# Kernel tuning notes

Hardware: AMD Instinct MI355X
Metric: run time of the kernel (lower is better)

## Reference

```python
import jax, jax.numpy as jnp
import numpy as np

EMBED = 50
SEQ = 100
NLABEL = 15
HID = 20
VOCAB = 50000
BATCH = 8192


def gru_scan(xs, W, U, b, return_sequences):
    """Keras GRUCell (reset_after=True, gate order z,r,h).
    xs: (B, T, D). W: (D, 3H), U: (H, 3H), b: (2, 3H) [input bias, recurrent bias].
    """
    B = xs.shape[0]
    H = U.shape[0]
    bi, br = b[0], b[1]
    h0 = jnp.zeros((B, H), dtype=xs.dtype)

    def step(h, x_t):
        mx = x_t @ W + bi                      # (B, 3H)
        mh = h @ U + br                        # (B, 3H)
        xz, xr, xh = mx[:, :H], mx[:, H:2*H], mx[:, 2*H:]
        hz, hr, hh_ = mh[:, :H], mh[:, H:2*H], mh[:, 2*H:]
        z = jax.nn.sigmoid(xz + hz)
        r = jax.nn.sigmoid(xr + hr)
        hh = jnp.tanh(xh + r * hh_)
        h_new = z * h + (1.0 - z) * hh
        return h_new, h_new

    xs_t = jnp.swapaxes(xs, 0, 1)              # (T, B, D)
    h_last, hs = jax.lax.scan(step, h0, xs_t)
    if return_sequences:
        return jnp.swapaxes(hs, 0, 1)          # (B, T, H)
    return h_last                               # (B, H)


def setup_inputs() -> dict:
    key = jax.random.key(0)
    ks = jax.random.split(key, 9)
    s = 0.05
    return {
        "x": jax.random.randint(ks[0], (BATCH, SEQ), 0, VOCAB),
        "emb_table": jax.random.normal(ks[1], (VOCAB, EMBED), jnp.float32) * s,
        "W1": jax.random.normal(ks[2], (EMBED, 3 * HID), jnp.float32) * s,
        "U1": jax.random.normal(ks[3], (HID, 3 * HID), jnp.float32) * s,
        "b1": jnp.zeros((2, 3 * HID), jnp.float32),
        "W2": jax.random.normal(ks[4], (HID, 3 * HID), jnp.float32) * s,
        "U2": jax.random.normal(ks[5], (HID, 3 * HID), jnp.float32) * s,
        "b2": jnp.zeros((2, 3 * HID), jnp.float32),
        "Wd": jax.random.normal(ks[6], (HID, NLABEL), jnp.float32) * s,
        "bd": jnp.zeros((NLABEL,), jnp.float32),
        "drop_rate": 0,
    }


def reference(x, emb_table, W1, U1, b1, W2, U2, b2, Wd, bd, drop_rate):
    emb = emb_table[x]                               # (B, T, E)
    seq = gru_scan(emb, W1, U1, b1, return_sequences=True)   # (B, T, H)
    enc = gru_scan(seq, W2, U2, b2, return_sequences=False)  # (B, H)
    # drop_rate == 0 -> tf.nn.dropout is identity
    logits = enc @ Wd + bd                           # (B, 15)
    return logits
```

## Files before the change

### kernel.cpp

```cpp
#include <hip/hip_runtime.h>
#include <hip/hip_bf16.h>
#include <hip/hip_fp16.h>

#define SEQ_T 100
#define HID 20
#define EMB_D 50
#define VOCAB_N 50000
#define TABW 60
#define NTILE 3125
#define BBLK 782

typedef short sh8 __attribute__((ext_vector_type(8)));
typedef float f4  __attribute__((ext_vector_type(4)));

#define OFF_U1P 0
#define OFF_W2P 600
#define OFF_U2P 1200
#define OFF_B1  3600
#define OFF_B2  3720
#define OFF_WD  3840
#define OFF_BD  4140
#define OFF_TAB 4160

__device__ __forceinline__ float ldf(const void* p, int i, int isf) {
  return isf ? ((const float*)p)[i]
             : __bfloat162float(((const __hip_bfloat16*)p)[i]);
}
__device__ __forceinline__ short f2bf(float f) {
  unsigned u = __float_as_uint(f);
  u += 0x7fffu + ((u >> 16) & 1u);
  return (short)(u >> 16);
}
__device__ __forceinline__ float rdl(float v, int l) {
  return __uint_as_float(__builtin_amdgcn_readlane(__float_as_uint(v), l));
}
__device__ __forceinline__ int detect_isf(const void* emb) {
  uint4 dv = ((const uint4*)emb)[threadIdx.x & 63];
  int big = 0;
#pragma unroll
  for (int i = 0; i < 4; ++i) {
    unsigned w = ((const unsigned*)&dv)[i];
    big |= (((w >> 7) & 0xFF) >= 140) | (((w >> 23) & 0xFF) >= 140);
  }
  return (__ballot(big) != 0ull) ? 1 : 0;
}

__global__ __launch_bounds__(256) void build_table(
    const void* __restrict__ emb, const void* __restrict__ W1,
    const void* __restrict__ b1,
    const void* __restrict__ U1, const void* __restrict__ W2,
    const void* __restrict__ U2, const void* __restrict__ b2,
    const void* __restrict__ Wd, const void* __restrict__ bd,
    float* __restrict__ ws)
{
  const int isf = detect_isf(emb);
  if (blockIdx.x == 0) {
    const int t = threadIdx.x;
    unsigned* wsu = (unsigned*)ws;
    for (int i = t; i < 600; i += 256) {
      const int j = i / 10, p = i % 10;
      const int k0 = 2 * p, k1 = 2 * p + 1;
#define PK(M) ((unsigned)__half_as_ushort(__float2half_rn(ldf(M, k0 * 60 + j, isf))) | \
               ((unsigned)__half_as_ushort(__float2half_rn(ldf(M, k1 * 60 + j, isf))) << 16))
      wsu[OFF_U1P + i] = PK(U1);
      wsu[OFF_W2P + i] = PK(W2);
      wsu[OFF_U2P + i] = PK(U2);
#undef PK
    }
    for (int i = t; i < 120; i += 256) {
      ws[OFF_B1 + i] = ldf(b1, i, isf);
      ws[OFF_B2 + i] = ldf(b2, i, isf);
    }
    for (int i = t; i < 300; i += 256) ws[OFF_WD + i] = ldf(Wd, i, isf);
    for (int i = t; i < 15;  i += 256) ws[OFF_BD + i] = ldf(bd, i, isf);
  }

  const int L = threadIdx.x & 63, q = L >> 4, c = L & 15;
  const int wid = blockIdx.x * 4 + (threadIdx.x >> 6);
  float* __restrict__ tab = ws + OFF_TAB;

  __shared__ int4 sB[64][8];
  if (threadIdx.x < 64) {
#pragma unroll
    for (int nt = 0; nt < 4; ++nt) {
      const int col = nt * 16 + c;
      sh8 B0, B1;
#pragma unroll
      for (int jj = 0; jj < 8; ++jj) {
        const int k0 = q * 8 + jj, k1 = 32 + q * 8 + jj;
        B0[jj] = (col < TABW) ? f2bf(ldf(W1, k0 * TABW + col, isf)) : (short)0;
        B1[jj] = (col < TABW && k1 < EMB_D)
                     ? f2bf(ldf(W1, k1 * TABW + col, isf)) : (short)0;
      }
      sB[L][nt * 2]     = *(const int4*)&B0;
      sB[L][nt * 2 + 1] = *(const int4*)&B1;
    }
  }
  float bi[4];
#pragma unroll
  for (int nt = 0; nt < 4; ++nt) {
    const int col = nt * 16 + c;
    bi[nt] = (col < TABW) ? ldf(b1, col, isf) : 0.f;
  }
  __syncthreads();

  for (int tile = wid; tile < NTILE; tile += BBLK * 4) {
    const int v0 = tile * 16;
    sh8 A0, A1;
#pragma unroll
    for (int jj = 0; jj < 8; ++jj) { A0[jj] = 0; A1[jj] = 0; }
    if (!isf) {
      const unsigned short* eb = (const unsigned short*)emb;
      const size_t rb = (size_t)(v0 + c) * EMB_D;
#pragma unroll
      for (int i = 0; i < 4; ++i) {
        unsigned d = *(const unsigned*)(eb + rb + q * 8 + 2 * i);
        A0[2 * i] = (short)(d & 0xffff); A0[2 * i + 1] = (short)(d >> 16);
      }
      const int k1b = 32 + q * 8;
#pragma unroll
      for (int i = 0; i < 4; ++i) {
        const int k = k1b + 2 * i;
        if (k + 1 < EMB_D) {
          unsigned d = *(const unsigned*)(eb + rb + k);
          A1[2 * i] = (short)(d & 0xffff); A1[2 * i + 1] = (short)(d >> 16);
        }
      }
    } else {
      const float* ef = (const float*)emb;
      const size_t rb = (size_t)(v0 + c) * EMB_D;
#pragma unroll
      for (int jj = 0; jj < 8; ++jj) {
        const int k0 = q * 8 + jj, k1 = 32 + q * 8 + jj;
        A0[jj] = f2bf(ef[rb + k0]);
        A1[jj] = (k1 < EMB_D) ? f2bf(ef[rb + k1]) : (short)0;
      }
    }
#pragma unroll
    for (int nt = 0; nt < 4; ++nt) {
      int4 b0i = sB[L][nt * 2], b1i = sB[L][nt * 2 + 1];
      sh8 B0 = *(const sh8*)&b0i, B1 = *(const sh8*)&b1i;
      const int col = nt * 16 + c;
      f4 acc = { bi[nt], bi[nt], bi[nt], bi[nt] };
      acc = __builtin_amdgcn_mfma_f32_16x16x32_bf16(A0, B0, acc, 0, 0, 0);
      acc = __builtin_amdgcn_mfma_f32_16x16x32_bf16(A1, B1, acc, 0, 0, 0);
      if (col < TABW) {
#pragma unroll
        for (int r = 0; r < 4; ++r)
          tab[(size_t)(v0 + q * 4 + r) * TABW + col] = acc[r];
      }
    }
  }
}

__global__ __launch_bounds__(256, 8) void gru_main(
    const int* __restrict__ x, const float* __restrict__ ws,
    const void* __restrict__ emb, void* __restrict__ out)
{
  const int isf = detect_isf(emb);
  const int j = threadIdx.x & 63;
  const int e = __builtin_amdgcn_readfirstlane(blockIdx.x * 4 + (threadIdx.x >> 6));
  const int jc = j < TABW ? j : 0;

  const int* xr = x + (size_t)e * SEQ_T;
  const float* tab = ws + OFF_TAB;
  const int o1 = jc * 40;
  const int jc4 = jc * 4;
  const int a1 = ((j - 20) & 63) * 4;
  const int a2 = ((j + 40) & 63) * 4;
  const float br1 = ws[OFF_B1 + 60 + jc];
  const float bi2 = ws[OFF_B2 + jc];
  const float br2 = ws[OFF_B2 + 60 + jc];
  float h2out;

  asm volatile(
    "global_load_dwordx4 v[10:13], %[o1], %[wsp] offset:0\n\t"
    "global_load_dwordx4 v[14:17], %[o1], %[wsp] offset:16\n\t"
    "global_load_dwordx2 v[18:19], %[o1], %[wsp] offset:32\n\t"
    "v_add_u32 v44, 0x960, %[o1]\n\t"
    "v_add_u32 v45, 0x12c0, %[o1]\n\t"
    "global_load_dwordx4 v[20:23], v44, %[wsp] offset:0\n\t"
    "global_load_dwordx4 v[24:27], v44, %[wsp] offset:16\n\t"
    "global_load_dwordx2 v[28:29], v44, %[wsp] offset:32\n\t"
    "global_load_dwordx4 v[30:33], v45, %[wsp] offset:0\n\t"
    "global_load_dwordx4 v[34:37], v45, %[wsp] offset:16\n\t"
    "global_load_dwordx2 v[38:39], v45, %[wsp] offset:32\n\t"
    "s_mov_b64 s[20:21], 0\n\ts_mov_b64 s[22:23], 0\n\t"
    "s_mov_b64 s[24:25], 0\n\ts_mov_b64 s[26:27], 0\n\t"
    "s_mov_b64 s[28:29], 0\n\t"
    "s_mov_b64 s[30:31], 0\n\ts_mov_b64 s[32:33], 0\n\t"
    "s_mov_b64 s[34:35], 0\n\ts_mov_b64 s[36:37], 0\n\t"
    "s_mov_b64 s[38:39], 0\n\t"
    "v_mov_b32 v40, 0\n\t"
    "v_mov_b32 v41, 0\n\t"
    "s_load_dword s65, %[xp], 0x0\n\t"
    "s_load_dword s66, %[xp], 0x4\n\t"
    "s_waitcnt lgkmcnt(0)\n\t"
    "s_mul_i32 s65, s65, 240\n\t"
    "s_mul_i32 s66, s66, 240\n\t"
    "v_add_u32 v50, s65, %[jc4]\n\t"
    "global_load_dword v42, v50, %[tabp]\n\t"
    "v_add_u32 v50, s66, %[jc4]\n\t"
    "global_load_dword v43, v50, %[tabp]\n\t"
    "s_load_dword s65, %[xp], 0x8\n\t"
    "s_movk_i32 s64, 0xc\n\t"
    "s_movk_i32 s67, 0x64\n\t"
    "s_waitcnt vmcnt(0)\n\t"
    "0:\n\t"
    "v_mov_b32 v44, %[br1]\n\t"
    "v_dot2_f32_f16 v44, s20, v10, v44\n\t"
    "v_dot2_f32_f16 v44, s21, v11, v44\n\t"
    "v_dot2_f32_f16 v44, s22, v12, v44\n\t"
    "v_dot2_f32_f16 v44, s23, v13, v44\n\t"
    "v_dot2_f32_f16 v44, s24, v14, v44\n\t"
    "v_dot2_f32_f16 v44, s25, v15, v44\n\t"
    "v_dot2_f32_f16 v44, s26, v16, v44\n\t"
    "v_dot2_f32_f16 v44, s27, v17, v44\n\t"
    "v_dot2_f32_f16 v44, s28, v18, v44\n\t"
    "v_dot2_f32_f16 v44, s29, v19, v44\n\t"
    "v_add_f32 v45, v42, v44\n\t"
    "v_mul_f32 v45, 0xbfb8aa3b, v45\n\t"
    "v_exp_f32 v45, v45\n\t"
    "s_nop 1\n\t"
    "v_add_f32 v45, 1.0, v45\n\t"
    "v_rcp_f32 v45, v45\n\t"
    "s_nop 1\n\t"
    "ds_bpermute_b32 v46, %[a1], v45\n\t"
    "s_waitcnt lgkmcnt(0)\n\t"
    "v_fma_f32 v47, v46, v44, v42\n\t"
    "v_mul_f32 v47, 0x4038aa3b, v47\n\t"
    "v_exp_f32 v47, v47\n\t"
    "s_nop 1\n\t"
    "v_add_f32 v47, 1.0, v47\n\t"
    "v_rcp_f32 v47, v47\n\t"
    "s_nop 1\n\t"
    "v_fma_f32 v47, -2.0, v47, 1.0\n\t"
    "ds_bpermute_b32 v46, %[a2], v47\n\t"
    "s_waitcnt lgkmcnt(0)\n\t"
    "v_sub_f32 v48, v40, v46\n\t"
    "v_fma_f32 v40, v45, v48, v46\n\t"
    "s_nop 1\n\t"
    "v_cvt_f16_f32 v46, v40\n\t"
    "s_nop 1\n\t"
    "ds_swizzle_b32 v47, v46 offset:0x041F\n\t"
    "s_waitcnt lgkmcnt(0)\n\t"
    "v_pack_b32_f16 v46, v46, v47\n\t"
    "s_nop 1\n\t"
    "v_readlane_b32 s20, v46, 0\n\t"
    "v_readlane_b32 s21, v46, 2\n\t"
    "v_readlane_b32 s22, v46, 4\n\t"
    "v_readlane_b32 s23, v46, 6\n\t"
    "v_readlane_b32 s24, v46, 8\n\t"
    "v_readlane_b32 s25, v46, 10\n\t"
    "v_readlane_b32 s26, v46, 12\n\t"
    "v_readlane_b32 s27, v46, 14\n\t"
    "v_readlane_b32 s28, v46, 16\n\t"
    "v_readlane_b32 s29, v46, 18\n\t"
    "s_mul_i32 s66, s65, 240\n\t"
    "v_add_u32 v50, s66, %[jc4]\n\t"
    "s_waitcnt vmcnt(0)\n\t"
    "v_mov_b32 v42, v43\n\t"
    "global_load_dword v43, v50, %[tabp]\n\t"
    "s_min_u32 s64, s64, 396\n\t"
    "s_load_dword s65, %[xp], s64\n\t"
    "s_add_u32 s64, s64, 4\n\t"
    "v_mov_b32 v44, %[bi2]\n\t"
    "v_mov_b32 v48, %[br2]\n\t"
    "v_dot2_f32_f16 v44, s20, v20, v44\n\t"
    "v_dot2_f32_f16 v48, s30, v30, v48\n\t"
    "v_dot2_f32_f16 v44, s21, v21, v44\n\t"
    "v_dot2_f32_f16 v48, s31, v31, v48\n\t"
    "v_dot2_f32_f16 v44, s22, v22, v44\n\t"
    "v_dot2_f32_f16 v48, s32, v32, v48\n\t"
    "v_dot2_f32_f16 v44, s23, v23, v44\n\t"
    "v_dot2_f32_f16 v48, s33, v33, v48\n\t"
    "v_dot2_f32_f16 v44, s24, v24, v44\n\t"
    "v_dot2_f32_f16 v48, s34, v34, v48\n\t"
    "v_dot2_f32_f16 v44, s25, v25, v44\n\t"
    "v_dot2_f32_f16 v48, s35, v35, v48\n\t"
    "v_dot2_f32_f16 v44, s26, v26, v44\n\t"
    "v_dot2_f32_f16 v48, s36, v36, v48\n\t"
    "v_dot2_f32_f16 v44, s27, v27, v44\n\t"
    "v_dot2_f32_f16 v48, s37, v37, v48\n\t"
    "v_dot2_f32_f16 v44, s28, v28, v44\n\t"
    "v_dot2_f32_f16 v48, s38, v38, v48\n\t"
    "v_dot2_f32_f16 v44, s29, v29, v44\n\t"
    "v_dot2_f32_f16 v48, s39, v39, v48\n\t"
    "v_add_f32 v45, v44, v48\n\t"
    "v_mul_f32 v45, 0xbfb8aa3b, v45\n\t"
    "v_exp_f32 v45, v45\n\t"
    "s_nop 1\n\t"
    "v_add_f32 v45, 1.0, v45\n\t"
    "v_rcp_f32 v45, v45\n\t"
    "s_nop 1\n\t"
    "ds_bpermute_b32 v46, %[a1], v45\n\t"
    "s_waitcnt lgkmcnt(0)\n\t"
    "v_fma_f32 v47, v46, v48, v44\n\t"
    "v_mul_f32 v47, 0x4038aa3b, v47\n\t"
    "v_exp_f32 v47, v47\n\t"
    "s_nop 1\n\t"
    "v_add_f32 v47, 1.0, v47\n\t"
    "v_rcp_f32 v47, v47\n\t"
    "s_nop 1\n\t"
    "v_fma_f32 v47, -2.0, v47, 1.0\n\t"
    "ds_bpermute_b32 v46, %[a2], v47\n\t"
    "s_waitcnt lgkmcnt(0)\n\t"
    "v_sub_f32 v49, v41, v46\n\t"
    "v_fma_f32 v41, v45, v49, v46\n\t"
    "s_nop 1\n\t"
    "v_cvt_f16_f32 v46, v41\n\t"
    "s_nop 1\n\t"
    "ds_swizzle_b32 v47, v46 offset:0x041F\n\t"
    "s_waitcnt lgkmcnt(0)\n\t"
    "v_pack_b32_f16 v46, v46, v47\n\t"
    "s_nop 1\n\t"
    "v_readlane_b32 s30, v46, 0\n\t"
    "v_readlane_b32 s31, v46, 2\n\t"
    "v_readlane_b32 s32, v46, 4\n\t"
    "v_readlane_b32 s33, v46, 6\n\t"
    "v_readlane_b32 s34, v46, 8\n\t"
    "v_readlane_b32 s35, v46, 10\n\t"
    "v_readlane_b32 s36, v46, 12\n\t"
    "v_readlane_b32 s37, v46, 14\n\t"
    "v_readlane_b32 s38, v46, 16\n\t"
    "v_readlane_b32 s39, v46, 18\n\t"
    "s_sub_u32 s67, s67, 1\n\t"
    "s_cmp_lg_u32 s67, 0\n\t"
    "s_cbranch_scc1 0b\n\t"
    "s_waitcnt vmcnt(0) lgkmcnt(0)\n\t"
    "v_mov_b32 %[h2o], v41\n\t"
    : [h2o] "=v"(h2out)
    : [wsp] "s"(ws), [xp] "s"(xr), [tabp] "s"(tab),
      [o1] "v"(o1), [jc4] "v"(jc4), [a1] "v"(a1), [a2] "v"(a2),
      [br1] "v"(br1), [bi2] "v"(bi2), [br2] "v"(br2)
    : "memory", "vcc", "scc",
      "v10","v11","v12","v13","v14","v15","v16","v17","v18","v19",
      "v20","v21","v22","v23","v24","v25","v26","v27","v28","v29",
      "v30","v31","v32","v33","v34","v35","v36","v37","v38","v39",
      "v40","v41","v42","v43","v44","v45","v46","v47","v48","v49","v50",
      "s20","s21","s22","s23","s24","s25","s26","s27","s28","s29",
      "s30","s31","s32","s33","s34","s35","s36","s37","s38","s39",
      "s64","s65","s66","s67");

  if (j < 15) {
    float a = ws[OFF_BD + j];
#pragma unroll
    for (int k = 0; k < HID; ++k)
      a = fmaf(rdl(h2out, k), ws[OFF_WD + k * 15 + j], a);
    if (isf) ((float*)out)[(size_t)e * 15 + j] = a;
    else ((__hip_bfloat16*)out)[(size_t)e * 15 + j] = __float2bfloat16(a);
  }
}

extern "C" void kernel_launch(void* const* d_in, const int* in_sizes, int n_in,
                              void* d_out, int out_size, void* d_ws, size_t ws_size,
                              hipStream_t stream) {
  const int* x    = (const int*)d_in[0];
  const void* emb = d_in[1];
  const void* W1  = d_in[2];
  const void* U1  = d_in[3];
  const void* b1  = d_in[4];
  const void* W2  = d_in[5];
  const void* U2  = d_in[6];
  const void* b2  = d_in[7];
  const void* Wd  = d_in[8];
  const void* bd  = d_in[9];
  float* ws = (float*)d_ws;

  build_table<<<BBLK, 256, 0, stream>>>(
      emb, W1, b1, U1, W2, U2, b2, Wd, bd, ws);
  gru_main<<<2048, 256, 0, stream>>>(x, ws, emb, d_out);
}
```

Baseline: 240.6 us.

## Software-pipeline GRU layers by one timestep and interleave both layers' gate math

Restructures the hand-written assembly loop so layer 1 at step t+1 and layer 2 at step t run together in one iteration. It adds a prologue step and unrolls the loop by two, with double-buffered scalar hidden-state registers. The two independent dependency chains are interleaved, including the dot products, exp/rcp, permutes and swizzles. This is meant to hide transcendental, LDS and readlane latency and to remove s_nop padding. The cost is extra SGPR/VGPR use and more complex embedding-load prefetch bookkeeping, with a risk of off-by-one errors in the epilogue and index handling.

Result: faster. 232.7 us (-3.3%).

```diff
diff --git a/kernel.cpp b/kernel.cpp
--- a/kernel.cpp
+++ b/kernel.cpp
@@ -191,34 +191,45 @@
     "s_mov_b64 s[30:31], 0\n\ts_mov_b64 s[32:33], 0\n\t"
     "s_mov_b64 s[34:35], 0\n\ts_mov_b64 s[36:37], 0\n\t"
     "s_mov_b64 s[38:39], 0\n\t"
+    "s_mov_b64 s[40:41], 0\n\ts_mov_b64 s[42:43], 0\n\t"
+    "s_mov_b64 s[44:45], 0\n\ts_mov_b64 s[46:47], 0\n\t"
+    "s_mov_b64 s[48:49], 0\n\t"
+    "s_mov_b64 s[50:51], 0\n\ts_mov_b64 s[52:53], 0\n\t"
+    "s_mov_b64 s[54:55], 0\n\ts_mov_b64 s[56:57], 0\n\t"
+    "s_mov_b64 s[58:59], 0\n\t"
     "v_mov_b32 v40, 0\n\t"
     "v_mov_b32 v41, 0\n\t"
     "s_load_dword s65, %[xp], 0x0\n\t"
     "s_load_dword s66, %[xp], 0x4\n\t"
+    "s_load_dword s68, %[xp], 0x8\n\t"
     "s_waitcnt lgkmcnt(0)\n\t"
     "s_mul_i32 s65, s65, 240\n\t"
     "s_mul_i32 s66, s66, 240\n\t"
+    "s_mul_i32 s68, s68, 240\n\t"
     "v_add_u32 v50, s65, %[jc4]\n\t"
+    "global_load_dword v53, v50, %[tabp]\n\t"
+    "v_add_u32 v50, s66, %[jc4]\n\t"
     "global_load_dword v42, v50, %[tabp]\n\t"
-    "v_add_u32 v50, s66, %[jc4]\n\t"
+    "v_add_u32 v50, s68, %[jc4]\n\t"
     "global_load_dword v43, v50, %[tabp]\n\t"
-    "s_load_dword s65, %[xp], 0x8\n\t"
-    "s_movk_i32 s64, 0xc\n\t"
-    "s_movk_i32 s67, 0x64\n\t"
-    "s_waitcnt vmcnt(0)\n\t"
-    "0:\n\t"
+    "s_load_dword s65, %[xp], 0xc\n\t"
+    "s_load_dword s68, %[xp], 0x10\n\t"
+    "s_movk_i32 s64, 0x14\n\t"
+    "s_movk_i32 s69, 0x18\n\t"
+    "s_movk_i32 s67, 0x32\n\t"
+    "s_waitcnt vmcnt(2)\n\t"
     "v_mov_b32 v44, %[br1]\n\t"
-    "v_dot2_f32_f16 v44, s20, v10, v44\n\t"
-    "v_dot2_f32_f16 v44, s21, v11, v44\n\t"
-    "v_dot2_f32_f16 v44, s22, v12, v44\n\t"
-    "v_dot2_f32_f16 v44, s23, v13, v44\n\t"
-    "v_dot2_f32_f16 v44, s24, v14, v44\n\t"
-    "v_dot2_f32_f16 v44, s25, v15, v44\n\t"
-    "v_dot2_f32_f16 v44, s26, v16, v44\n\t"
-    "v_dot2_f32_f16 v44, s27, v17, v44\n\t"
-    "v_dot2_f32_f16 v44, s28, v18, v44\n\t"
-    "v_dot2_f32_f16 v44, s29, v19, v44\n\t"
-    "v_add_f32 v45, v42, v44\n\t"
+    "v_dot2_f32_f16 v44, s40, v10, v44\n\t"
+    "v_dot2_f32_f16 v44, s41, v11, v44\n\t"
+    "v_dot2_f32_f16 v44, s42, v12, v44\n\t"
+    "v_dot2_f32_f16 v44, s43, v13, v44\n\t"
+    "v_dot2_f32_f16 v44, s44, v14, v44\n\t"
+    "v_dot2_f32_f16 v44, s45, v15, v44\n\t"
+    "v_dot2_f32_f16 v44, s46, v16, v44\n\t"
+    "v_dot2_f32_f16 v44, s47, v17, v44\n\t"
+    "v_dot2_f32_f16 v44, s48, v18, v44\n\t"
+    "v_dot2_f32_f16 v44, s49, v19, v44\n\t"
+    "v_add_f32 v45, v53, v44\n\t"
     "v_mul_f32 v45, 0xbfb8aa3b, v45\n\t"
     "v_exp_f32 v45, v45\n\t"
     "s_nop 1\n\t"
@@ -227,7 +238,7 @@
     "s_nop 1\n\t"
     "ds_bpermute_b32 v46, %[a1], v45\n\t"
     "s_waitcnt lgkmcnt(0)\n\t"
-    "v_fma_f32 v47, v46, v44, v42\n\t"
+    "v_fma_f32 v47, v46, v44, v53\n\t"
     "v_mul_f32 v47, 0x4038aa3b, v47\n\t"
     "v_exp_f32 v47, v47\n\t"
     "s_nop 1\n\t"
@@ -256,74 +267,207 @@
     "v_readlane_b32 s27, v46, 14\n\t"
     "v_readlane_b32 s28, v46, 16\n\t"
     "v_readlane_b32 s29, v46, 18\n\t"
+    "0:\n\t"
+    "v_mov_b32 v44, %[br1]\n\t"
+    "v_mov_b32 v51, %[bi2]\n\t"
+    "v_mov_b32 v52, %[br2]\n\t"
+    "v_dot2_f32_f16 v44, s20, v10, v44\n\t"
+    "v_dot2_f32_f16 v51, s20, v20, v51\n\t"
+    "v_dot2_f32_f16 v52, s50, v30, v52\n\t"
+    "v_dot2_f32_f16 v44, s21, v11, v44\n\t"
+    "v_dot2_f32_f16 v51, s21, v21, v51\n\t"
+    "v_dot2_f32_f16 v52, s51, v31, v52\n\t"
+    "v_dot2_f32_f16 v44, s22, v12, v44\n\t"
+    "v_dot2_f32_f16 v51, s22, v22, v51\n\t"
+    "v_dot2_f32_f16 v52, s52, v32, v52\n\t"
+    "v_dot2_f32_f16 v44, s23, v13, v44\n\t"
+    "v_dot2_f32_f16 v51, s23, v23, v51\n\t"
+    "v_dot2_f32_f16 v52, s53, v33, v52\n\t"
+    "v_dot2_f32_f16 v44, s24, v14, v44\n\t"
+    "v_dot2_f32_f16 v51, s24, v24, v51\n\t"
+    "v_dot2_f32_f16 v52, s54, v34, v52\n\t"
+    "v_dot2_f32_f16 v44, s25, v15, v44\n\t"
+    "v_dot2_f32_f16 v51, s25, v25, v51\n\t"
+    "v_dot2_f32_f16 v52, s55, v35, v52\n\t"
+    "v_dot2_f32_f16 v44, s26, v16, v44\n\t"
+    "v_dot2_f32_f16 v51, s26, v26, v51\n\t"
+    "v_dot2_f32_f16 v52, s56, v36, v52\n\t"
+    "v_dot2_f32_f16 v44, s27, v17, v44\n\t"
+    "v_dot2_f32_f16 v51, s27, v27, v51\n\t"
+    "v_dot2_f32_f16 v52, s57, v37, v52\n\t"
+    "v_dot2_f32_f16 v44, s28, v18, v44\n\t"
+    "v_dot2_f32_f16 v51, s28, v28, v51\n\t"
+    "v_dot2_f32_f16 v52, s58, v38, v52\n\t"
+    "v_dot2_f32_f16 v44, s29, v19, v44\n\t"
+    "v_dot2_f32_f16 v51, s29, v29, v51\n\t"
+    "v_dot2_f32_f16 v52, s59, v39, v52\n\t"
+    "s_waitcnt vmcnt(1)\n\t"
+    "v_add_f32 v45, v42, v44\n\t"
+    "v_add_f32 v53, v51, v52\n\t"
+    "v_mul_f32 v45, 0xbfb8aa3b, v45\n\t"
+    "v_mul_f32 v53, 0xbfb8aa3b, v53\n\t"
+    "v_exp_f32 v45, v45\n\t"
+    "v_exp_f32 v53, v53\n\t"
+    "v_add_f32 v45, 1.0, v45\n\t"
+    "v_add_f32 v53, 1.0, v53\n\t"
+    "v_rcp_f32 v45, v45\n\t"
+    "v_rcp_f32 v53, v53\n\t"
+    "ds_bpermute_b32 v46, %[a1], v45\n\t"
+    "ds_bpermute_b32 v54, %[a1], v53\n\t"
     "s_mul_i32 s66, s65, 240\n\t"
     "v_add_u32 v50, s66, %[jc4]\n\t"
-    "s_waitcnt vmcnt(0)\n\t"
-    "v_mov_b32 v42, v43\n\t"
-    "global_load_dword v43, v50, %[tabp]\n\t"
+    "s_waitcnt lgkmcnt(0)\n\t"
+    "v_fma_f32 v47, v46, v44, v42\n\t"
+    "v_fma_f32 v55, v54, v52, v51\n\t"
+    "global_load_dword v42, v50, %[tabp]\n\t"
+    "v_mul_f32 v47, 0x4038aa3b, v47\n\t"
+    "v_mul_f32 v55, 0x4038aa3b, v55\n\t"
+    "v_exp_f32 v47, v47\n\t"
+    "v_exp_f32 v55, v55\n\t"
+    "v_add_f32 v47, 1.0, v47\n\t"
+    "v_add_f32 v55, 1.0, v55\n\t"
+    "v_rcp_f32 v47, v47\n\t"
+    "v_rcp_f32 v55, v55\n\t"
+    "v_fma_f32 v47, -2.0, v47, 1.0\n\t"
+    "v_fma_f32 v55, -2.0, v55, 1.0\n\t"
+    "ds_bpermute_b32 v46, %[a2], v47\n\t"
+    "ds_bpermute_b32 v54, %[a2], v55\n\t"
+    "s_waitcnt lgkmcnt(0)\n\t"
+    "v_sub_f32 v48, v40, v46\n\t"
+    "v_sub_f32 v51, v41, v54\n\t"
+    "v_fma_f32 v40, v45, v48, v46\n\t"
+    "v_fma_f32 v41, v53, v51, v54\n\t"
+    "v_cvt_f16_f32 v46, v40\n\t"
+    "v_cvt_f16_f32 v54, v41\n\t"
+    "ds_swizzle_b32 v47, v46 offset:0x041F\n\t"
+    "ds_swizzle_b32 v55, v54 offset:0x041F\n\t"
+    "s_waitcnt lgkmcnt(0)\n\t"
+    "v_pack_b32_f16 v46, v46, v47\n\t"
+    "v_pack_b32_f16 v54, v54, v55\n\t"
     "s_min_u32 s64, s64, 396\n\t"
     "s_load_dword s65, %[xp], s64\n\t"
-    "s_add_u32 s64, s64, 4\n\t"
-    "v_mov_b32 v44, %[bi2]\n\t"
-    "v_mov_b32 v48, %[br2]\n\t"
-    "v_dot2_f32_f16 v44, s20, v20, v44\n\t"
-    "v_dot2_f32_f16 v48, s30, v30, v48\n\t"
-    "v_dot2_f32_f16 v44, s21, v21, v44\n\t"
-    "v_dot2_f32_f16 v48, s31, v31, v48\n\t"
-    "v_dot2_f32_f16 v44, s22, v22, v44\n\t"
-    "v_dot2_f32_f16 v48, s32, v32, v48\n\t"
-    "v_dot2_f32_f16 v44, s23, v23, v44\n\t"
-    "v_dot2_f32_f16 v48, s33, v33, v48\n\t"
-    "v_dot2_f32_f16 v44, s24, v24, v44\n\t"
-    "v_dot2_f32_f16 v48, s34, v34, v48\n\t"
-    "v_dot2_f32_f16 v44, s25, v25, v44\n\t"
-    "v_dot2_f32_f16 v48, s35, v35, v48\n\t"
-    "v_dot2_f32_f16 v44, s26, v26, v44\n\t"
-    "v_dot2_f32_f16 v48, s36, v36, v48\n\t"
-    "v_dot2_f32_f16 v44, s27, v27, v44\n\t"
-    "v_dot2_f32_f16 v48, s37, v37, v48\n\t"
-    "v_dot2_f32_f16 v44, s28, v28, v44\n\t"
-    "v_dot2_f32_f16 v48, s38, v38, v48\n\t"
-    "v_dot2_f32_f16 v44, s29, v29, v44\n\t"
-    "v_dot2_f32_f16 v48, s39, v39, v48\n\t"
-    "v_add_f32 v45, v44, v48\n\t"
+    "s_add_u32 s64, s64, 8\n\t"
+    "s_nop 0\n\t"
+    "v_readlane_b32 s40, v46, 0\n\t"
+    "v_readlane_b32 s41, v46, 2\n\t"
+    "v_readlane_b32 s42, v46, 4\n\t"
+    "v_readlane_b32 s43, v46, 6\n\t"
+    "v_readlane_b32 s44, v46, 8\n\t"
+    "v_readlane_b32 s45, v46, 10\n\t"
+    "v_readlane_b32 s46, v46, 12\n\t"
+    "v_readlane_b32 s47, v46, 14\n\t"
+    "v_readlane_b32 s48, v46, 16\n\t"
+    "v_readlane_b32 s49, v46, 18\n\t"
+    "v_readlane_b32 s30, v54, 0\n\t"
+    "v_readlane_b32 s31, v54, 2\n\t"
+    "v_readlane_b32 s32, v54, 4\n\t"
+    "v_readlane_b32 s33, v54, 6\n\t"
+    "v_readlane_b32 s34, v54, 8\n\t"
+    "v_readlane_b32 s35, v54, 10\n\t"
+    "v_readlane_b32 s36, v54, 12\n\t"
+    "v_readlane_b32 s37, v54, 14\n\t"
+    "v_readlane_b32 s38, v54, 16\n\t"
+    "v_readlane_b32 s39, v54, 18\n\t"
+    "v_mov_b32 v44, %[br1]\n\t"
+    "v_mov_b32 v51, %[bi2]\n\t"
+    "v_mov_b32 v52, %[br2]\n\t"
+    "v_dot2_f32_f16 v44, s40, v10, v44\n\t"
+    "v_dot2_f32_f16 v51, s40, v20, v51\n\t"
+    "v_dot2_f32_f16 v52, s30, v30, v52\n\t"
+    "v_dot2_f32_f16 v44, s41, v11, v44\n\t"
+    "v_dot2_f32_f16 v51, s41, v21, v51\n\t"
+    "v_dot2_f32_f16 v52, s31, v31, v52\n\t"
+    "v_dot2_f32_f16 v44, s42, v12, v44\n\t"
+    "v_dot2_f32_f16 v51, s42, v22, v51\n\t"
+    "v_dot2_f32_f16 v52, s32, v32, v52\n\t"
+    "v_dot2_f32_f16 v44, s43, v13, v44\n\t"
+    "v_dot2_f32_f16 v51, s43, v23, v51\n\t"
+    "v_dot2_f32_f16 v52, s33, v33, v52\n\t"
+    "v_dot2_f32_f16 v44, s44, v14, v44\n\t"
+    "v_dot2_f32_f16 v51, s44, v24, v51\n\t"
+    "v_dot2_f32_f16 v52, s34, v34, v52\n\t"
+    "v_dot2_f32_f16 v44, s45, v15, v44\n\t"
+    "v_dot2_f32_f16 v51, s45, v25, v51\n\t"
+    "v_dot2_f32_f16 v52, s35, v35, v52\n\t"
+    "v_dot2_f32_f16 v44, s46, v16, v44\n\t"
+    "v_dot2_f32_f16 v51, s46, v26, v51\n\t"
+    "v_dot2_f32_f16 v52, s36, v36, v52\n\t"
+    "v_dot2_f32_f16 v44, s47, v17, v44\n\t"
+    "v_dot2_f32_f16 v51, s47, v27, v51\n\t"
+    "v_dot2_f32_f16 v52, s37, v37, v52\n\t"
+    "v_dot2_f32_f16 v44, s48, v18, v44\n\t"
+    "v_dot2_f32_f16 v51, s48, v28, v51\n\t"
+    "v_dot2_f32_f16 v52, s38, v38, v52\n\t"
+    "v_dot2_f32_f16 v44, s49, v19, v44\n\t"
+    "v_dot2_f32_f16 v51, s49, v29, v51\n\t"
+    "v_dot2_f32_f16 v52, s39, v39, v52\n\t"
+    "s_waitcnt vmcnt(1)\n\t"
+    "v_add_f32 v45, v43, v44\n\t"
+    "v_add_f32 v53, v51, v52\n\t"
     "v_mul_f32 v45, 0xbfb8aa3b, v45\n\t"
+    "v_mul_f32 v53, 0xbfb8aa3b, v53\n\t"
     "v_exp_f32 v45, v45\n\t"
-    "s_nop 1\n\t"
+    "v_exp_f32 v53, v53\n\t"
     "v_add_f32 v45, 1.0, v45\n\t"
+    "v_add_f32 v53, 1.0, v53\n\t"
     "v_rcp_f32 v45, v45\n\t"
-    "s_nop 1\n\t"
+    "v_rcp_f32 v53, v53\n\t"
     "ds_bpermute_b32 v46, %[a1], v45\n\t"
-    "s_waitcnt lgkmcnt(0)\n\t"
-    "v_fma_f32 v47, v46, v48, v44\n\t"
+    "ds_bpermute_b32 v54, %[a1], v53\n\t"
+    "s_mul_i32 s66, s68, 240\n\t"
+    "v_add_u32 v50, s66, %[jc4]\n\t"
+    "s_waitcnt lgkmcnt(0)\n\t"
+    "v_fma_f32 v47, v46, v44, v43\n\t"
+    "v_fma_f32 v55, v54, v52, v51\n\t"
+    "global_load_dword v43, v50, %[tabp]\n\t"
     "v_mul_f32 v47, 0x4038aa3b, v47\n\t"
+    "v_mul_f32 v55, 0x4038aa3b, v55\n\t"
     "v_exp_f32 v47, v47\n\t"
-    "s_nop 1\n\t"
+    "v_exp_f32 v55, v55\n\t"
     "v_add_f32 v47, 1.0, v47\n\t"
+    "v_add_f32 v55, 1.0, v55\n\t"
     "v_rcp_f32 v47, v47\n\t"
-    "s_nop 1\n\t"
+    "v_rcp_f32 v55, v55\n\t"
     "v_fma_f32 v47, -2.0, v47, 1.0\n\t"
+    "v_fma_f32 v55, -2.0, v55, 1.0\n\t"
     "ds_bpermute_b32 v46, %[a2], v47\n\t"
-    "s_waitcnt lgkmcnt(0)\n\t"
-    "v_sub_f32 v49, v41, v46\n\t"
-    "v_fma_f32 v41, v45, v49, v46\n\t"
-    "s_nop 1\n\t"
-    "v_cvt_f16_f32 v46, v41\n\t"
-    "s_nop 1\n\t"
+    "ds_bpermute_b32 v54, %[a2], v55\n\t"
+    "s_waitcnt lgkmcnt(0)\n\t"
+    "v_sub_f32 v48, v40, v46\n\t"
+    "v_sub_f32 v51, v41, v54\n\t"
+    "v_fma_f32 v40, v45, v48, v46\n\t"
+    "v_fma_f32 v41, v53, v51, v54\n\t"
+    "v_cvt_f16_f32 v46, v40\n\t"
+    "v_cvt_f16_f32 v54, v41\n\t"
     "ds_swizzle_b32 v47, v46 offset:0x041F\n\t"
+    "ds_swizzle_b32 v55, v54 offset:0x041F\n\t"
     "s_waitcnt lgkmcnt(0)\n\t"
     "v_pack_b32_f16 v46, v46, v47\n\t"
-    "s_nop 1\n\t"
-    "v_readlane_b32 s30, v46, 0\n\t"
-    "v_readlane_b32 s31, v46, 2\n\t"
-    "v_readlane_b32 s32, v46, 4\n\t"
-    "v_readlane_b32 s33, v46, 6\n\t"
-    "v_readlane_b32 s34, v46, 8\n\t"
-    "v_readlane_b32 s35, v46, 10\n\t"
-    "v_readlane_b32 s36, v46, 12\n\t"
-    "v_readlane_b32 s37, v46, 14\n\t"
-    "v_readlane_b32 s38, v46, 16\n\t"
-    "v_readlane_b32 s39, v46, 18\n\t"
+    "v_pack_b32_f16 v54, v54, v55\n\t"
+    "s_min_u32 s69, s69, 392\n\t"
+    "s_load_dword s68, %[xp], s69\n\t"
+    "s_add_u32 s69, s69, 8\n\t"
+    "s_nop 0\n\t"
+    "v_readlane_b32 s20, v46, 0\n\t"
+    "v_readlane_b32 s21, v46, 2\n\t"
+    "v_readlane_b32 s22, v46, 4\n\t"
+    "v_readlane_b32 s23, v46, 6\n\t"
+    "v_readlane_b32 s24, v46, 8\n\t"
+    "v_readlane_b32 s25, v46, 10\n\t"
+    "v_readlane_b32 s26, v46, 12\n\t"
+    "v_readlane_b32 s27, v46, 14\n\t"
+    "v_readlane_b32 s28, v46, 16\n\t"
+    "v_readlane_b32 s29, v46, 18\n\t"
+    "v_readlane_b32 s50, v54, 0\n\t"
+    "v_readlane_b32 s51, v54, 2\n\t"
+    "v_readlane_b32 s52, v54, 4\n\t"
+    "v_readlane_b32 s53, v54, 6\n\t"
+    "v_readlane_b32 s54, v54, 8\n\t"
+    "v_readlane_b32 s55, v54, 10\n\t"
+    "v_readlane_b32 s56, v54, 12\n\t"
+    "v_readlane_b32 s57, v54, 14\n\t"
+    "v_readlane_b32 s58, v54, 16\n\t"
+    "v_readlane_b32 s59, v54, 18\n\t"
     "s_sub_u32 s67, s67, 1\n\t"
     "s_cmp_lg_u32 s67, 0\n\t"
     "s_cbranch_scc1 0b\n\t"
@@ -338,9 +482,12 @@
       "v20","v21","v22","v23","v24","v25","v26","v27","v28","v29",
       "v30","v31","v32","v33","v34","v35","v36","v37","v38","v39",
       "v40","v41","v42","v43","v44","v45","v46","v47","v48","v49","v50",
+      "v51","v52","v53","v54","v55",
       "s20","s21","s22","s23","s24","s25","s26","s27","s28","s29",
       "s30","s31","s32","s33","s34","s35","s36","s37","s38","s39",
-      "s64","s65","s66","s67");
+      "s40","s41","s42","s43","s44","s45","s46","s47","s48","s49",
+      "s50","s51","s52","s53","s54","s55","s56","s57","s58","s59",
+      "s64","s65","s66","s67","s68","s69");
 
   if (j < 15) {
     float a = ws[OFF_BD + j];
```
